# Kernel optimization log

Measured on AMD Instinct MI355X. Metric: run time of the kernel, lower is better.

## Reference

```python
import jax, jax.numpy as jnp
import numpy as np
import math

# Static multi-level spatial layout (H, W) per level and flattened start offsets.
SHAPES = ((100, 100), (50, 50), (25, 25), (13, 13))
STARTS = (0, 10000, 12500, 13125)
LEN_IN = 13294
D_MODEL, N_LEVELS, N_HEADS, N_POINTS = 256, 4, 8, 4
D_HEAD = D_MODEL // N_HEADS
B, LQ = 2, 13294


def _offset_bias():
    # Replicates MSDeformAttn._reset_parameters radial grid init for sampling_offsets.bias
    thetas = np.arange(N_HEADS, dtype=np.float32) * (2.0 * math.pi / N_HEADS)
    grid = np.stack([np.cos(thetas), np.sin(thetas)], axis=-1)  # [nh, 2]
    grid = grid / np.abs(grid).max(axis=-1, keepdims=True)
    # [nh, nl, np, 2] with per-point radius (i+1)
    full = np.tile(grid[:, None, None, :], (1, N_LEVELS, N_POINTS, 1))
    full = full * np.arange(1, N_POINTS + 1, dtype=np.float32)[None, None, :, None]
    return full.reshape(-1)


def setup_inputs() -> dict:
    key = jax.random.key(0)
    ks = jax.random.split(key, 8)
    xavier = 1.0 / math.sqrt(D_MODEL)
    return {
        "query": jax.random.normal(ks[0], (B, LQ, D_MODEL), jnp.float32),
        "reference_points": jax.random.uniform(ks[1], (B, LQ, N_LEVELS, 2), jnp.float32),
        "input_flatten": jax.random.normal(ks[2], (B, LEN_IN, D_MODEL), jnp.float32),
        "input_spatial_shapes": jnp.array(SHAPES, jnp.int32),
        "input_level_start_index": jnp.array(STARTS, jnp.int32),
        "W_off": jax.random.normal(ks[3], (D_MODEL, N_HEADS * N_LEVELS * N_POINTS * 2), jnp.float32) * 0.01,
        "b_off": jnp.asarray(_offset_bias()),
        "W_attn": jax.random.normal(ks[4], (D_MODEL, N_HEADS * N_LEVELS * N_POINTS), jnp.float32) * 0.02,
        "b_attn": jnp.zeros((N_HEADS * N_LEVELS * N_POINTS,), jnp.float32),
        "W_val": jax.random.normal(ks[5], (D_MODEL, D_MODEL), jnp.float32) * xavier,
        "b_val": jnp.zeros((D_MODEL,), jnp.float32),
        "W_out": jax.random.normal(ks[6], (D_MODEL, D_MODEL), jnp.float32) * xavier,
        "b_out": jnp.zeros((D_MODEL,), jnp.float32),
    }


def reference(query, reference_points, input_flatten, input_spatial_shapes,
              input_level_start_index, W_off, b_off, W_attn, b_attn,
              W_val, b_val, W_out, b_out):
    Bq, Lq, _ = query.shape
    value = (input_flatten @ W_val + b_val).reshape(Bq, LEN_IN, N_HEADS, D_HEAD)

    off = (query @ W_off + b_off).reshape(Bq, Lq, N_HEADS, N_LEVELS, N_POINTS, 2)
    aw = (query @ W_attn + b_attn).reshape(Bq, Lq, N_HEADS, N_LEVELS * N_POINTS)
    aw = jax.nn.softmax(aw, axis=-1).reshape(Bq, Lq, N_HEADS, N_LEVELS, N_POINTS)

    # offset normalizer is (W, H) per level
    normalizer = jnp.array([[w, h] for (h, w) in SHAPES], query.dtype)  # [nl, 2]
    loc = reference_points[:, :, None, :, None, :] + off / normalizer[None, None, None, :, None, :]

    bi = jnp.arange(Bq)[:, None, None, None]
    hi = jnp.arange(N_HEADS)[None, None, :, None]
    out = jnp.zeros((Bq, Lq, N_HEADS, D_HEAD), query.dtype)

    # Per-level zero-padded bilinear sampling (math-equivalent to grid_sample
    # align_corners=False, padding_mode='zeros' on the padded max_H x max_W grid,
    # since the padded region is zero-filled).
    for lvl, (H, W) in enumerate(SHAPES):
        s = STARTS[lvl]
        vflat = value[:, s:s + H * W]  # [B, H*W, nh, dh]
        l = loc[:, :, :, lvl]          # [B, Lq, nh, P, 2] in normalized coords
        x = l[..., 0] * W - 0.5
        y = l[..., 1] * H - 0.5
        x0 = jnp.floor(x)
        y0 = jnp.floor(y)
        sampled = jnp.zeros((Bq, Lq, N_HEADS, N_POINTS, D_HEAD), query.dtype)
        for dx in (0, 1):
            for dy in (0, 1):
                xi = x0 + dx
                yi = y0 + dy
                wgt = (1.0 - jnp.abs(x - xi)) * (1.0 - jnp.abs(y - yi))
                valid = (xi >= 0) & (xi <= W - 1) & (yi >= 0) & (yi <= H - 1)
                idx = (jnp.clip(yi, 0, H - 1) * W + jnp.clip(xi, 0, W - 1)).astype(jnp.int32)
                v = vflat[bi, idx, hi]  # [B, Lq, nh, P, dh]
                sampled = sampled + v * (wgt * valid)[..., None]
        out = out + jnp.einsum('bqhpd,bqhp->bqhd', sampled, aw[:, :, :, lvl])

    out = out.reshape(Bq, Lq, D_MODEL)
    return out @ W_out + b_out
```

## Files before the change

kernel.cpp:

```cpp
#include <hip/hip_runtime.h>
#include <math.h>

#define BQ 2
#define LQ 13294
#define LEN_IN 13294
#define M_ROWS 26588

__device__ __constant__ int c_HW[4]    = {100, 50, 25, 13};
__device__ __constant__ int c_START[4] = {0, 10000, 12500, 13125};

typedef __attribute__((ext_vector_type(8))) short bf16x8;
typedef __attribute__((ext_vector_type(4))) float f32x4;
typedef __attribute__((ext_vector_type(2))) float f32x2;

__device__ inline unsigned short f2bf(float f) {
  union { float f; unsigned int u; } x; x.f = f;
  unsigned int u = x.u;
  return (unsigned short)((u + 0x7fffu + ((u >> 16) & 1u)) >> 16);
}
__device__ inline float h2f(unsigned short h) {
  _Float16 x; __builtin_memcpy(&x, &h, 2); return (float)x;
}
__device__ inline unsigned short f2h(float f) {
  _Float16 x = (_Float16)f; unsigned short u; __builtin_memcpy(&u, &x, 2); return u;
}

__device__ inline void gl_lds16(const void* g, void* l) {
  __builtin_amdgcn_global_load_lds(
      (const __attribute__((address_space(1))) unsigned int*)g,
      (__attribute__((address_space(3))) unsigned int*)l, 16, 0, 0);
}

#define CONV_BLKS 3456
#define N4EACH (M_ROWS * 64)

__global__ __launch_bounds__(256) void prep_all(
    const float* __restrict__ query, const float* __restrict__ inpf,
    const float* __restrict__ W_off, const float* __restrict__ b_off,
    const float* __restrict__ W_attn, const float* __restrict__ b_attn,
    const float* __restrict__ W_val, const float* __restrict__ W_out,
    unsigned short* __restrict__ q_bf, unsigned short* __restrict__ in_bf,
    unsigned short* __restrict__ Wval_t, unsigned short* __restrict__ Woa_t,
    unsigned short* __restrict__ Wout_t, float* __restrict__ b_oa) {
  const int bx = blockIdx.x;
  if (bx < CONV_BLKS) {
    int i = bx * 256 + threadIdx.x;
    const int stride = CONV_BLKS * 256;
    for (; i < 2 * N4EACH; i += stride) {
      const float* src; unsigned short* dst; int j;
      if (i < N4EACH) { src = query; dst = q_bf; j = i; }
      else            { src = inpf;  dst = in_bf; j = i - N4EACH; }
      const float4 v = ((const float4*)src)[j];
      ushort4 h;
      h.x = f2bf(v.x); h.y = f2bf(v.y); h.z = f2bf(v.z); h.w = f2bf(v.w);
      ((ushort4*)dst)[j] = h;
    }
    return;
  }
  const int idx = (bx - CONV_BLKS) * 256 + threadIdx.x;
  const int SZ1 = 256 * 256;
  const int SZ2 = 384 * 256;
  if (idx < SZ1) {
    const int n = idx >> 8, k = idx & 255;
    Wval_t[idx] = f2bf(W_val[k * 256 + n]);
  } else if (idx < SZ1 + SZ2) {
    const int j = idx - SZ1;
    const int n = j >> 8, k = j & 255;
    const float v = (n < 256) ? W_off[k * 256 + n] : W_attn[k * 128 + (n - 256)];
    Woa_t[j] = f2bf(v);
  } else {
    const int j = idx - SZ1 - SZ2;
    const int n = j >> 8, k = j & 255;
    Wout_t[j] = f2bf(W_out[k * 256 + n]);
  }
  if (bx == CONV_BLKS) b_oa[threadIdx.x] = b_off[threadIdx.x];
  if (bx == CONV_BLKS + 1 && threadIdx.x < 128)
    b_oa[256 + threadIdx.x] = b_attn[threadIdx.x];
}

template <int CT>
__global__ __launch_bounds__(256) void gemm_mfma(
    const unsigned short* __restrict__ A, const unsigned short* __restrict__ Wt,
    const float* __restrict__ bias, void* __restrict__ Cp, int M, int N) {
  __shared__ unsigned short As[128 * 64];
  __shared__ unsigned short Bs[128 * 64];
  const int tid = threadIdx.x;
  const int wv = tid >> 6;
  const int lane = tid & 63;
  const int m0 = blockIdx.x * 128;
  const int n0 = blockIdx.y * 128;
  const int wm = (wv & 1) * 64;
  const int wn = (wv >> 1) * 64;
  const int fr = lane & 15;
  const int fq = lane >> 4;
  const int lr = lane >> 3;
  const int gch = (lane & 7) ^ lr;

  const unsigned short* ga[4];
  const unsigned short* gb[4];
#pragma unroll
  for (int t = 0; t < 4; ++t) {
    int ar = m0 + wv * 32 + t * 8 + lr;
    if (ar > M - 1) ar = M - 1;
    ga[t] = A + (size_t)ar * 256 + gch * 8;
    gb[t] = Wt + (size_t)(n0 + wv * 32 + t * 8 + lr) * 256 + gch * 8;
  }

  f32x4 acc[4][4];
#pragma unroll
  for (int i = 0; i < 4; ++i)
#pragma unroll
    for (int j = 0; j < 4; ++j) acc[i][j] = (f32x4){0.f, 0.f, 0.f, 0.f};

  for (int k0 = 0; k0 < 256; k0 += 64) {
    __syncthreads();
#pragma unroll
    for (int t = 0; t < 4; ++t) {
      gl_lds16(ga[t], &As[(wv * 32 + t * 8) * 64]);
      gl_lds16(gb[t], &Bs[(wv * 32 + t * 8) * 64]);
      ga[t] += 64; gb[t] += 64;
    }
    __syncthreads();
#pragma unroll
    for (int kk = 0; kk < 2; ++kk) {
      bf16x8 af[4], bf[4];
#pragma unroll
      for (int i = 0; i < 4; ++i) {
        const int row = wm + i * 16 + fr;
        af[i] = *(const bf16x8*)&As[row * 64 + ((kk * 4 + fq) ^ (row & 7)) * 8];
      }
#pragma unroll
      for (int j = 0; j < 4; ++j) {
        const int row = wn + j * 16 + fr;
        bf[j] = *(const bf16x8*)&Bs[row * 64 + ((kk * 4 + fq) ^ (row & 7)) * 8];
      }
#pragma unroll
      for (int i = 0; i < 4; ++i)
#pragma unroll
        for (int j = 0; j < 4; ++j)
          acc[i][j] = __builtin_amdgcn_mfma_f32_16x16x32_bf16(af[i], bf[j],
                                                              acc[i][j], 0, 0, 0);
    }
  }

  const int col = fr;
  const int row0 = fq * 4;
#pragma unroll
  for (int i = 0; i < 4; ++i) {
#pragma unroll
    for (int j = 0; j < 4; ++j) {
      const int gn = n0 + wn + j * 16 + col;
      const float bb = bias[gn];
#pragma unroll
      for (int r = 0; r < 4; ++r) {
        const int gm = m0 + wm + i * 16 + row0 + r;
        if (gm < M) {
          const float v = acc[i][j][r] + bb;
          if (CT == 1)
            ((unsigned short*)Cp)[(size_t)gm * N + gn] = f2bf(v);
          else if (CT == 2)
            ((unsigned short*)Cp)[(size_t)gm * N + gn] = f2h(v);
          else
            ((float*)Cp)[(size_t)gm * N + gn] = v;
        }
      }
    }
  }
}

__global__ __launch_bounds__(256) void sample_kernel(
    const float* __restrict__ refp,
    const unsigned short* __restrict__ oa,
    const unsigned short* __restrict__ value,
    unsigned int* __restrict__ mid) {
  const int tid = threadIdx.x;
  const int q0 = blockIdx.x * 4;

  __shared__ float2 s_wo[4][4][136];

  {
    const int pid = tid & 127;
    const int h = pid >> 4;
    const int lp = pid & 15;
    const int l = lp >> 2;
    const int p = lp & 3;
    const int HW = c_HW[l];
    const float fW = (float)HW;
    const int sub = tid >> 7;
#pragma unroll
    for (int qq = 0; qq < 2; ++qq) {
      const int qi = sub * 2 + qq;
      const int q = q0 + qi;
      const int b = (q >= LQ) ? 1 : 0;

      const float logit = h2f(oa[(size_t)q * 384 + 256 + pid]);
      float mx = logit;
#pragma unroll
      for (int s = 1; s < 16; s <<= 1) mx = fmaxf(mx, __shfl_xor(mx, s, 16));
      const float e = expf(logit - mx);
      float sum = e;
#pragma unroll
      for (int s = 1; s < 16; s <<= 1) sum += __shfl_xor(sum, s, 16);
      const float a = e / sum;

      const unsigned int opk =
          *(const unsigned int*)&oa[(size_t)q * 384 + h * 32 + l * 8 + p * 2];
      const float ox = h2f((unsigned short)(opk & 0xffffu));
      const float oy = h2f((unsigned short)(opk >> 16));
      const float rx = refp[((size_t)q * 4 + l) * 2 + 0];
      const float ry = refp[((size_t)q * 4 + l) * 2 + 1];
      const float x = (rx + ox / fW) * fW - 0.5f;
      const float y = (ry + oy / fW) * fW - 0.5f;
      const float x0 = floorf(x);
      const float y0 = floorf(y);

#pragma unroll
      for (int t = 0; t < 4; ++t) {
        const int dx = t & 1;
        const int dy = t >> 1;
        const float xi = x0 + (float)dx;
        const float yi = y0 + (float)dy;
        const float wgt = (1.0f - fabsf(x - xi)) * (1.0f - fabsf(y - yi));
        const bool valid =
            (xi >= 0.f) && (xi <= fW - 1.f) && (yi >= 0.f) && (yi <= fW - 1.f);
        int xc = (int)xi; xc = xc < 0 ? 0 : (xc > HW - 1 ? HW - 1 : xc);
        int yc = (int)yi; yc = yc < 0 ? 0 : (yc > HW - 1 ? HW - 1 : yc);
        const int row = b * LEN_IN + c_START[l] + yc * HW + xc;
        float2 wo;
        wo.x = valid ? wgt * a : 0.f;
        wo.y = __int_as_float(row * 512 + h * 64);
        s_wo[qi][t][h * 17 + lp] = wo;
      }
    }
  }
  __syncthreads();

  {
    const int qi = tid >> 6;
    const int g = tid & 63;
    const int h = g >> 3;
    const int dp8 = g & 7;
    const int q = q0 + qi;
    const char* vbase = (const char*)value + dp8 * 8;
    f32x2 acc0 = {0.f, 0.f}, acc1 = {0.f, 0.f};
#pragma unroll 4
    for (int lp = 0; lp < 16; ++lp) {
      const int si = h * 17 + lp;
#pragma unroll
      for (int t = 0; t < 4; ++t) {
        const float2 f = s_wo[qi][t][si];
        const uint2 v = *(const uint2*)(vbase + __float_as_int(f.y));
        f32x2 av0 = {__uint_as_float(v.x << 16),
                     __uint_as_float(v.x & 0xffff0000u)};
        f32x2 av1 = {__uint_as_float(v.y << 16),
                     __uint_as_float(v.y & 0xffff0000u)};
        acc0 += f.x * av0;
        acc1 += f.x * av1;
      }
    }
    uint2 pk;
    pk.x = (unsigned int)f2bf(acc0.x) | ((unsigned int)f2bf(acc0.y) << 16);
    pk.y = (unsigned int)f2bf(acc1.x) | ((unsigned int)f2bf(acc1.y) << 16);
    *(uint2*)&mid[(size_t)q * 128 + h * 16 + dp8 * 2] = pk;
  }
}

extern "C" void kernel_launch(void* const* d_in, const int* in_sizes, int n_in,
                              void* d_out, int out_size, void* d_ws,
                              size_t ws_size, hipStream_t stream) {
  const float* query  = (const float*)d_in[0];
  const float* refp   = (const float*)d_in[1];
  const float* inpf   = (const float*)d_in[2];
  const float* W_off  = (const float*)d_in[5];
  const float* b_off  = (const float*)d_in[6];
  const float* W_attn = (const float*)d_in[7];
  const float* b_attn = (const float*)d_in[8];
  const float* W_val  = (const float*)d_in[9];
  const float* b_val  = (const float*)d_in[10];
  const float* W_out  = (const float*)d_in[11];
  const float* b_out  = (const float*)d_in[12];
  float* out = (float*)d_out;

  unsigned char* w = (unsigned char*)d_ws;
  unsigned short* Wval_t = (unsigned short*)w;  w += 256 * 256 * 2;
  unsigned short* Woa_t  = (unsigned short*)w;  w += 384 * 256 * 2;
  unsigned short* Wout_t = (unsigned short*)w;  w += 256 * 256 * 2;
  float*          b_oa   = (float*)w;           w += 384 * 4 + 64;
  unsigned short* q_bf   = (unsigned short*)w;  w += (size_t)M_ROWS * 256 * 2;
  unsigned short* in_bf  = (unsigned short*)w;  w += (size_t)M_ROWS * 256 * 2;
  unsigned short* v_buf  = (unsigned short*)w;  w += (size_t)M_ROWS * 256 * 2;
  unsigned short* oa_buf = (unsigned short*)w;  w += (size_t)M_ROWS * 384 * 2;
  unsigned int*   mid_buf = (unsigned int*)w;

  const dim3 blk(256);
  const int mg = (M_ROWS + 127) / 128;

  prep_all<<<dim3(CONV_BLKS + 896), blk, 0, stream>>>(
      query, inpf, W_off, b_off, W_attn, b_attn, W_val, W_out,
      q_bf, in_bf, Wval_t, Woa_t, Wout_t, b_oa);
  gemm_mfma<1><<<dim3(mg, 2), blk, 0, stream>>>(in_bf, Wval_t, b_val, v_buf,
                                                M_ROWS, 256);
  gemm_mfma<2><<<dim3(mg, 3), blk, 0, stream>>>(q_bf, Woa_t, b_oa, oa_buf,
                                                M_ROWS, 384);
  sample_kernel<<<dim3(M_ROWS / 4), blk, 0, stream>>>(refp, oa_buf, v_buf,
                                                      mid_buf);
  gemm_mfma<0><<<dim3(mg, 2), blk, 0, stream>>>((const unsigned short*)mid_buf,
                                                Wout_t, b_out, out, M_ROWS, 256);
}
```

Before: 223.8 us.

## Fuse value and offset GEMMs, vectorize GEMM epilogue, retile sampling to two queries

The value projection and the offset/attention projection now run as a single launch whose grid's y dimension selects which GEMM each block does, removing one kernel launch and its tail. The MFMA operands are swapped so each lane holds four consecutive output columns, which lets the epilogue write float4 or packed 4x16-bit stores with a vectorized bias load instead of scalar stores. The sampling kernel now handles two queries per block with one thread per query-point, and each gather thread reads 4 bytes instead of 8. This doubles the grid size and the number of gather instructions, trading per-thread work for more parallelism.

Result: faster. 214.2 us (-4.3%).

```diff
diff --git a/kernel.cpp b/kernel.cpp
--- a/kernel.cpp
+++ b/kernel.cpp
@@ -11,7 +11,6 @@
 
 typedef __attribute__((ext_vector_type(8))) short bf16x8;
 typedef __attribute__((ext_vector_type(4))) float f32x4;
-typedef __attribute__((ext_vector_type(2))) float f32x2;
 
 __device__ inline unsigned short f2bf(float f) {
   union { float f; unsigned int u; } x; x.f = f;
@@ -79,16 +78,14 @@
 }
 
 template <int CT>
-__global__ __launch_bounds__(256) void gemm_mfma(
+__device__ inline void gemm_body(
     const unsigned short* __restrict__ A, const unsigned short* __restrict__ Wt,
-    const float* __restrict__ bias, void* __restrict__ Cp, int M, int N) {
-  __shared__ unsigned short As[128 * 64];
-  __shared__ unsigned short Bs[128 * 64];
+    const float* __restrict__ bias, void* __restrict__ Cp,
+    int M, int N, int m0, int n0,
+    unsigned short* As, unsigned short* Bs) {
   const int tid = threadIdx.x;
   const int wv = tid >> 6;
   const int lane = tid & 63;
-  const int m0 = blockIdx.x * 128;
-  const int n0 = blockIdx.y * 128;
   const int wm = (wv & 1) * 64;
   const int wn = (wv >> 1) * 64;
   const int fr = lane & 15;
@@ -138,34 +135,68 @@
       for (int i = 0; i < 4; ++i)
 #pragma unroll
         for (int j = 0; j < 4; ++j)
-          acc[i][j] = __builtin_amdgcn_mfma_f32_16x16x32_bf16(af[i], bf[j],
+          acc[i][j] = __builtin_amdgcn_mfma_f32_16x16x32_bf16(bf[j], af[i],
                                                               acc[i][j], 0, 0, 0);
     }
   }
 
-  const int col = fr;
-  const int row0 = fq * 4;
-#pragma unroll
-  for (int i = 0; i < 4; ++i) {
-#pragma unroll
-    for (int j = 0; j < 4; ++j) {
-      const int gn = n0 + wn + j * 16 + col;
-      const float bb = bias[gn];
-#pragma unroll
-      for (int r = 0; r < 4; ++r) {
-        const int gm = m0 + wm + i * 16 + row0 + r;
-        if (gm < M) {
-          const float v = acc[i][j][r] + bb;
-          if (CT == 1)
-            ((unsigned short*)Cp)[(size_t)gm * N + gn] = f2bf(v);
-          else if (CT == 2)
-            ((unsigned short*)Cp)[(size_t)gm * N + gn] = f2h(v);
-          else
-            ((float*)Cp)[(size_t)gm * N + gn] = v;
-        }
+#pragma unroll
+  for (int j = 0; j < 4; ++j) {
+    const int nb = n0 + wn + j * 16 + fq * 4;
+    const float4 b4 = *(const float4*)&bias[nb];
+#pragma unroll
+    for (int i = 0; i < 4; ++i) {
+      const int m = m0 + wm + i * 16 + fr;
+      if (m >= M) continue;
+      const float v0 = acc[i][j][0] + b4.x;
+      const float v1 = acc[i][j][1] + b4.y;
+      const float v2 = acc[i][j][2] + b4.z;
+      const float v3 = acc[i][j][3] + b4.w;
+      if (CT == 0) {
+        float4 o = make_float4(v0, v1, v2, v3);
+        *(float4*)&((float*)Cp)[(size_t)m * N + nb] = o;
+      } else if (CT == 1) {
+        uint2 o;
+        o.x = (unsigned int)f2bf(v0) | ((unsigned int)f2bf(v1) << 16);
+        o.y = (unsigned int)f2bf(v2) | ((unsigned int)f2bf(v3) << 16);
+        *(uint2*)&((unsigned short*)Cp)[(size_t)m * N + nb] = o;
+      } else {
+        uint2 o;
+        o.x = (unsigned int)f2h(v0) | ((unsigned int)f2h(v1) << 16);
+        o.y = (unsigned int)f2h(v2) | ((unsigned int)f2h(v3) << 16);
+        *(uint2*)&((unsigned short*)Cp)[(size_t)m * N + nb] = o;
       }
     }
   }
+}
+
+__global__ __launch_bounds__(256) void gemm_fused(
+    const unsigned short* __restrict__ in_bf,
+    const unsigned short* __restrict__ q_bf,
+    const unsigned short* __restrict__ Wval_t,
+    const unsigned short* __restrict__ Woa_t,
+    const float* __restrict__ b_val, const float* __restrict__ b_oa,
+    void* __restrict__ v_buf, void* __restrict__ oa_buf) {
+  __shared__ unsigned short As[128 * 64];
+  __shared__ unsigned short Bs[128 * 64];
+  const int m0 = blockIdx.x * 128;
+  if (blockIdx.y < 2) {
+    gemm_body<1>(in_bf, Wval_t, b_val, v_buf, M_ROWS, 256,
+                 m0, blockIdx.y * 128, As, Bs);
+  } else {
+    gemm_body<2>(q_bf, Woa_t, b_oa, oa_buf, M_ROWS, 384,
+                 m0, (blockIdx.y - 2) * 128, As, Bs);
+  }
+}
+
+__global__ __launch_bounds__(256) void gemm_out(
+    const unsigned short* __restrict__ mid,
+    const unsigned short* __restrict__ Wout_t,
+    const float* __restrict__ b_out, float* __restrict__ out) {
+  __shared__ unsigned short As[128 * 64];
+  __shared__ unsigned short Bs[128 * 64];
+  gemm_body<0>(mid, Wout_t, b_out, out, M_ROWS, 256,
+               blockIdx.x * 128, blockIdx.y * 128, As, Bs);
 }
 
 __global__ __launch_bounds__(256) void sample_kernel(
@@ -174,9 +205,11 @@
     const unsigned short* __restrict__ value,
     unsigned int* __restrict__ mid) {
   const int tid = threadIdx.x;
-  const int q0 = blockIdx.x * 4;
-
-  __shared__ float2 s_wo[4][4][136];
+  const int qi = tid >> 7;
+  const int q = blockIdx.x * 2 + qi;
+  const int b = (q >= LQ) ? 1 : 0;
+
+  __shared__ float2 s_wo[2][4][136];
 
   {
     const int pid = tid & 127;
@@ -186,82 +219,67 @@
     const int p = lp & 3;
     const int HW = c_HW[l];
     const float fW = (float)HW;
-    const int sub = tid >> 7;
-#pragma unroll
-    for (int qq = 0; qq < 2; ++qq) {
-      const int qi = sub * 2 + qq;
-      const int q = q0 + qi;
-      const int b = (q >= LQ) ? 1 : 0;
-
-      const float logit = h2f(oa[(size_t)q * 384 + 256 + pid]);
-      float mx = logit;
-#pragma unroll
-      for (int s = 1; s < 16; s <<= 1) mx = fmaxf(mx, __shfl_xor(mx, s, 16));
-      const float e = expf(logit - mx);
-      float sum = e;
-#pragma unroll
-      for (int s = 1; s < 16; s <<= 1) sum += __shfl_xor(sum, s, 16);
-      const float a = e / sum;
-
-      const unsigned int opk =
-          *(const unsigned int*)&oa[(size_t)q * 384 + h * 32 + l * 8 + p * 2];
-      const float ox = h2f((unsigned short)(opk & 0xffffu));
-      const float oy = h2f((unsigned short)(opk >> 16));
-      const float rx = refp[((size_t)q * 4 + l) * 2 + 0];
-      const float ry = refp[((size_t)q * 4 + l) * 2 + 1];
-      const float x = (rx + ox / fW) * fW - 0.5f;
-      const float y = (ry + oy / fW) * fW - 0.5f;
-      const float x0 = floorf(x);
-      const float y0 = floorf(y);
-
-#pragma unroll
-      for (int t = 0; t < 4; ++t) {
-        const int dx = t & 1;
-        const int dy = t >> 1;
-        const float xi = x0 + (float)dx;
-        const float yi = y0 + (float)dy;
-        const float wgt = (1.0f - fabsf(x - xi)) * (1.0f - fabsf(y - yi));
-        const bool valid =
-            (xi >= 0.f) && (xi <= fW - 1.f) && (yi >= 0.f) && (yi <= fW - 1.f);
-        int xc = (int)xi; xc = xc < 0 ? 0 : (xc > HW - 1 ? HW - 1 : xc);
-        int yc = (int)yi; yc = yc < 0 ? 0 : (yc > HW - 1 ? HW - 1 : yc);
-        const int row = b * LEN_IN + c_START[l] + yc * HW + xc;
-        float2 wo;
-        wo.x = valid ? wgt * a : 0.f;
-        wo.y = __int_as_float(row * 512 + h * 64);
-        s_wo[qi][t][h * 17 + lp] = wo;
-      }
+
+    const float logit = h2f(oa[(size_t)q * 384 + 256 + pid]);
+    float mx = logit;
+#pragma unroll
+    for (int s = 1; s < 16; s <<= 1) mx = fmaxf(mx, __shfl_xor(mx, s, 16));
+    const float e = expf(logit - mx);
+    float sum = e;
+#pragma unroll
+    for (int s = 1; s < 16; s <<= 1) sum += __shfl_xor(sum, s, 16);
+    const float a = e / sum;
+
+    const unsigned int opk =
+        *(const unsigned int*)&oa[(size_t)q * 384 + h * 32 + l * 8 + p * 2];
+    const float ox = h2f((unsigned short)(opk & 0xffffu));
+    const float oy = h2f((unsigned short)(opk >> 16));
+    const float rx = refp[((size_t)q * 4 + l) * 2 + 0];
+    const float ry = refp[((size_t)q * 4 + l) * 2 + 1];
+    const float x = (rx + ox / fW) * fW - 0.5f;
+    const float y = (ry + oy / fW) * fW - 0.5f;
+    const float x0 = floorf(x);
+    const float y0 = floorf(y);
+
+#pragma unroll
+    for (int t = 0; t < 4; ++t) {
+      const int dx = t & 1;
+      const int dy = t >> 1;
+      const float xi = x0 + (float)dx;
+      const float yi = y0 + (float)dy;
+      const float wgt = (1.0f - fabsf(x - xi)) * (1.0f - fabsf(y - yi));
+      const bool valid =
+          (xi >= 0.f) && (xi <= fW - 1.f) && (yi >= 0.f) && (yi <= fW - 1.f);
+      int xc = (int)xi; xc = xc < 0 ? 0 : (xc > HW - 1 ? HW - 1 : xc);
+      int yc = (int)yi; yc = yc < 0 ? 0 : (yc > HW - 1 ? HW - 1 : yc);
+      const int row = b * LEN_IN + c_START[l] + yc * HW + xc;
+      float2 wo;
+      wo.x = valid ? wgt * a : 0.f;
+      wo.y = __int_as_float(row * 512 + h * 64);
+      s_wo[qi][t][h * 17 + lp] = wo;
     }
   }
   __syncthreads();
 
   {
-    const int qi = tid >> 6;
-    const int g = tid & 63;
-    const int h = g >> 3;
-    const int dp8 = g & 7;
-    const int q = q0 + qi;
-    const char* vbase = (const char*)value + dp8 * 8;
-    f32x2 acc0 = {0.f, 0.f}, acc1 = {0.f, 0.f};
+    const int g = tid & 127;
+    const int h = g >> 4;
+    const int dp = g & 15;
+    const char* vbase = (const char*)value + dp * 4;
+    float acc0 = 0.f, acc1 = 0.f;
 #pragma unroll 4
     for (int lp = 0; lp < 16; ++lp) {
       const int si = h * 17 + lp;
 #pragma unroll
       for (int t = 0; t < 4; ++t) {
         const float2 f = s_wo[qi][t][si];
-        const uint2 v = *(const uint2*)(vbase + __float_as_int(f.y));
-        f32x2 av0 = {__uint_as_float(v.x << 16),
-                     __uint_as_float(v.x & 0xffff0000u)};
-        f32x2 av1 = {__uint_as_float(v.y << 16),
-                     __uint_as_float(v.y & 0xffff0000u)};
-        acc0 += f.x * av0;
-        acc1 += f.x * av1;
+        const unsigned int v = *(const unsigned int*)(vbase + __float_as_int(f.y));
+        acc0 += f.x * __uint_as_float(v << 16);
+        acc1 += f.x * __uint_as_float(v & 0xffff0000u);
       }
     }
-    uint2 pk;
-    pk.x = (unsigned int)f2bf(acc0.x) | ((unsigned int)f2bf(acc0.y) << 16);
-    pk.y = (unsigned int)f2bf(acc1.x) | ((unsigned int)f2bf(acc1.y) << 16);
-    *(uint2*)&mid[(size_t)q * 128 + h * 16 + dp8 * 2] = pk;
+    mid[(size_t)q * 128 + h * 16 + dp] =
+        (unsigned int)f2bf(acc0) | ((unsigned int)f2bf(acc1) << 16);
   }
 }
 
@@ -298,12 +316,10 @@
   prep_all<<<dim3(CONV_BLKS + 896), blk, 0, stream>>>(
       query, inpf, W_off, b_off, W_attn, b_attn, W_val, W_out,
       q_bf, in_bf, Wval_t, Woa_t, Wout_t, b_oa);
-  gemm_mfma<1><<<dim3(mg, 2), blk, 0, stream>>>(in_bf, Wval_t, b_val, v_buf,
-                                                M_ROWS, 256);
-  gemm_mfma<2><<<dim3(mg, 3), blk, 0, stream>>>(q_bf, Woa_t, b_oa, oa_buf,
-                                                M_ROWS, 384);
-  sample_kernel<<<dim3(M_ROWS / 4), blk, 0, stream>>>(refp, oa_buf, v_buf,
+  gemm_fused<<<dim3(mg, 5), blk, 0, stream>>>(in_bf, q_bf, Wval_t, Woa_t,
+                                              b_val, b_oa, v_buf, oa_buf);
+  sample_kernel<<<dim3(M_ROWS / 2), blk, 0, stream>>>(refp, oa_buf, v_buf,
                                                       mid_buf);
-  gemm_mfma<0><<<dim3(mg, 2), blk, 0, stream>>>((const unsigned short*)mid_buf,
-                                                Wout_t, b_out, out, M_ROWS, 256);
-}
+  gemm_out<<<dim3(mg, 2), blk, 0, stream>>>((const unsigned short*)mid_buf,
+                                            Wout_t, b_out, out);
+}
```
